# Optimization experiments

Measured on AMD Instinct MI355X. Metric: run time of the kernel, lower is better.

The kernel has to match this reference:

```python
import jax, jax.numpy as jnp
import numpy as np

HEAD_NUM = 16


def setup_inputs() -> dict:
    key = jax.random.key(0)
    k1, k2, k3, k4 = jax.random.split(key, 4)
    B, S, E = 8, 1024, 1024
    inputs = jax.random.normal(k1, (B, S, E), dtype=jnp.float32)
    W_Query = jax.random.normal(k2, (E, E), dtype=jnp.float32) * 0.05
    W_Key = jax.random.normal(k3, (E, E), dtype=jnp.float32) * 0.05
    W_Value = jax.random.normal(k4, (E, E), dtype=jnp.float32) * 0.05
    return {"inputs": inputs, "W_Query": W_Query, "W_Key": W_Key, "W_Value": W_Value}


def reference(inputs, W_Query, W_Key, W_Value):
    B, S, E = inputs.shape
    H = HEAD_NUM
    D = E // H
    # QKV projections: [B,S,E] @ [E,E] -> [B,S,E]
    q = jnp.einsum('bse,ef->bsf', inputs, W_Query).reshape(B, S, H, D)
    k = jnp.einsum('bse,ef->bsf', inputs, W_Key).reshape(B, S, H, D)
    v = jnp.einsum('bse,ef->bsf', inputs, W_Value).reshape(B, S, H, D)
    # NOTE: original has NO 1/sqrt(D) scaling.
    scores = jnp.einsum('bihd,bjhd->bhij', q, k)  # [B,H,S,S]
    att = jax.nn.softmax(scores, axis=-1)
    out = jnp.einsum('bhij,bjhd->bihd', att, v).reshape(B, S, E)
    return jax.nn.relu(out)
```

## Files before the change

kernel.cpp:

```cpp
#include <hip/hip_runtime.h>
#include <cstdint>
#include <cstddef>

#define B_ 8
#define S_ 1024
#define E_ 1024
#define H_ 16
#define D_ 64
#define M_ (B_*S_)

typedef _Float16 f16;
typedef __attribute__((ext_vector_type(8))) _Float16 f16x8;
typedef __attribute__((ext_vector_type(4))) _Float16 f16x4;
typedef __attribute__((ext_vector_type(4))) float  f32x4;
typedef __attribute__((ext_vector_type(16))) float f32x16;
typedef __attribute__((ext_vector_type(4))) int    int4v;
typedef __attribute__((ext_vector_type(2))) int    int2v;

__device__ __forceinline__ f32x4 mfma16(f16x8 a, f16x8 b, f32x4 c) {
  return __builtin_amdgcn_mfma_f32_16x16x32_f16(a, b, c, 0, 0, 0);
}
__device__ __forceinline__ f32x16 mfma32(f16x8 a, f16x8 b, f32x16 c) {
  return __builtin_amdgcn_mfma_f32_32x32x16_f16(a, b, c, 0, 0, 0);
}
__device__ __forceinline__ void gll16(const f16* g, f16* l) {
  __builtin_amdgcn_global_load_lds(
      (const __attribute__((address_space(1))) void*)g,
      (__attribute__((address_space(3))) void*)l, 16, 0, 0);
}
__device__ __forceinline__ int pkrtz(float lo, float hi) {
  return __builtin_bit_cast(int, __builtin_amdgcn_cvt_pkrtz(lo, hi));
}

__global__ __launch_bounds__(256) void presplit_kernel(
    const float* __restrict__ X, f16* __restrict__ Xf) {
  size_t i = ((size_t)blockIdx.x * 256 + threadIdx.x) * 8;
  f32x4 v0 = *(const f32x4*)&X[i];
  f32x4 v1 = *(const f32x4*)&X[i + 4];
  f16x8 hv;
#pragma unroll
  for (int j = 0; j < 4; ++j) {
    hv[j] = (f16)v0[j];
    hv[j + 4] = (f16)v1[j];
  }
  *(f16x8*)&Xf[i] = hv;
}

__global__ __launch_bounds__(512) void wt_conv3_kernel(
    const float* __restrict__ Wq, const float* __restrict__ Wk,
    const float* __restrict__ Wv, f16* __restrict__ oq, f16* __restrict__ ok,
    f16* __restrict__ ov) {
  const float* W = blockIdx.z == 0 ? Wq : (blockIdx.z == 1 ? Wk : Wv);
  f16* o = blockIdx.z == 0 ? oq : (blockIdx.z == 1 ? ok : ov);
  const float scl = blockIdx.z == 0 ? 1.4426950408889634f : 1.0f;
  __shared__ float t[64][65];
  const int f0 = blockIdx.x * 64, e0 = blockIdx.y * 64;
  const int tx = threadIdx.x, ty = threadIdx.y;
#pragma unroll
  for (int j = 0; j < 8; ++j)
    t[ty + 8 * j][tx] = W[(size_t)(e0 + ty + 8 * j) * E_ + f0 + tx];
  __syncthreads();
#pragma unroll
  for (int j = 0; j < 8; ++j)
    o[(size_t)(f0 + ty + 8 * j) * E_ + e0 + tx] =
        (f16)(t[tx][ty + 8 * j] * scl);
}

__global__ __launch_bounds__(256) void gemm_qkv_kernel(
    const f16* __restrict__ Xf,
    const f16* __restrict__ Wq, const f16* __restrict__ Wk,
    const f16* __restrict__ Wv,
    f16* __restrict__ Qf, f16* __restrict__ Kf, f16* __restrict__ Vt) {
  __shared__ f16 sA[128][64], sB[128][64];
  const int bid = blockIdx.x;
  const int xcd = bid & 7, idx = bid >> 3;
  const int mb = xcd * 8 + idx / 24;
  const int nb = idx % 24;
  const int z = nb >> 3;
  const int n0 = (nb & 7) * 128, m0 = mb * 128;
  const f16* __restrict__ Bt = z == 0 ? Wq : (z == 1 ? Wk : Wv);
  const int tid = threadIdx.x;
  const int lane = tid & 63, w = tid >> 6;
  const int wm = (w >> 1) * 64, wn = (w & 1) * 64;
  const int fr = lane & 15, fg = lane >> 4;
  f32x4 acc[4][4] = {};
  for (int k0 = 0; k0 < E_; k0 += 64) {
#pragma unroll
    for (int i = 0; i < 4; ++i) {
      int ci = tid + i * 256;
      int r = ci >> 3, cl = ci & 7;
      int cs = (cl ^ (r & 7)) * 8;
      gll16(Xf + (size_t)(m0 + r) * E_ + k0 + cs, &sA[0][0] + ci * 8);
      gll16(Bt + (size_t)(n0 + r) * E_ + k0 + cs, &sB[0][0] + ci * 8);
    }
    __syncthreads();
#pragma unroll
    for (int kh2 = 0; kh2 < 2; ++kh2) {
      f16x8 ah[4];
#pragma unroll
      for (int mi = 0; mi < 4; ++mi) {
        int rA = wm + mi * 16 + fr;
        ah[mi] = *(const f16x8*)&sA[rA][(((kh2 * 4 + fg) ^ (rA & 7))) * 8];
      }
#pragma unroll
      for (int ni = 0; ni < 4; ++ni) {
        int rB = wn + ni * 16 + fr;
        f16x8 bh = *(const f16x8*)&sB[rB][(((kh2 * 4 + fg) ^ (rB & 7))) * 8];
#pragma unroll
        for (int mi = 0; mi < 4; ++mi)
          acc[mi][ni] = mfma16(ah[mi], bh, acc[mi][ni]);
      }
    }
    __syncthreads();
  }
  if (z < 2) {
    f16* Of = z == 0 ? Qf : Kf;
#pragma unroll
    for (int mi = 0; mi < 4; ++mi)
#pragma unroll
      for (int ni = 0; ni < 4; ++ni)
#pragma unroll
        for (int r = 0; r < 4; ++r) {
          int row = m0 + wm + mi * 16 + (lane >> 4) * 4 + r;
          int col = n0 + wn + ni * 16 + fr;
          int bb = row >> 10, s = row & 1023;
          int hd = col >> 6, d = col & 63;
          Of[((size_t)(bb * H_ + hd) * S_ + s) * D_ + d] = (f16)acc[mi][ni][r];
        }
  } else {
#pragma unroll
    for (int mi = 0; mi < 4; ++mi)
#pragma unroll
      for (int ni = 0; ni < 4; ++ni) {
        int row = m0 + wm + mi * 16 + (lane >> 4) * 4;
        int col = n0 + wn + ni * 16 + fr;
        int bb = row >> 10, s = row & 1023;
        int hd = col >> 6, d = col & 63;
        f16x4 p;
#pragma unroll
        for (int r = 0; r < 4; ++r) p[r] = (f16)acc[mi][ni][r];
        *(f16x4*)&Vt[((size_t)(bb * H_ + hd) * D_ + d) * S_ + s] = p;
      }
  }
}

__global__ __launch_bounds__(256, 4) void attn_kernel(
    const f16* __restrict__ Qf, const f16* __restrict__ Kf,
    const f16* __restrict__ Vt, float* __restrict__ out) {
  __shared__ f16 sK[2][64][64], sV[2][64][64];
  const int bid = blockIdx.x;
  const int bh = (bid & 7) * 16 + (bid >> 6);
  const int qb = (bid >> 3) & 7;
  const int hd = bh & 15, bb = bh >> 4;
  const int tid = threadIdx.x;
  const int lane = tid & 63, w = tid >> 6;
  const int cq = lane & 31, h = lane >> 5;
  const int rsw = cq & 7;
  const size_t base = (size_t)bh * (S_ * D_);
  const f16* Qf_p = Qf + base;
  const f16* Kf_p = Kf + base;
  const f16* Vt_p = Vt + base;
  const int q0 = qb * 128 + w * 32;

  f16x8 qh_[4];
#pragma unroll
  for (int ks = 0; ks < 4; ++ks)
    qh_[ks] = *(const f16x8*)&Qf_p[(size_t)(q0 + cq) * D_ + ks * 16 + 8 * h];

  f16x8 ones;
#pragma unroll
  for (int j = 0; j < 8; ++j) ones[j] = (f16)1.0f;

  float m_run;
  f32x16 O[2] = {}, Ol = {};
  f16x8 pf[4];

#define STAGE(buf, kb)                                                        \
  {                                                                           \
    _Pragma("unroll")                                                         \
    for (int half = 0; half < 2; ++half) {                                    \
      int ci = tid + half * 256;                                              \
      int row = ci >> 3, cl = ci & 7;                                         \
      int cs = cl ^ (row & 7);                                                \
      gll16(Kf_p + (size_t)((kb) + row) * D_ + cs * 8, &sK[buf][0][0] + ci * 8); \
      gll16(Vt_p + (size_t)row * S_ + (kb) + cs * 8, &sV[buf][0][0] + ci * 8);   \
    }                                                                         \
  }

#define QKT(scv, bufi)                                                        \
  {                                                                           \
    _Pragma("unroll")                                                         \
    for (int f = 0; f < 2; ++f) {                                             \
      _Pragma("unroll")                                                       \
      for (int ks = 0; ks < 4; ++ks) {                                        \
        int cc = ((2 * ks + h) ^ rsw) * 8;                                    \
        f16x8 kv = *(const f16x8*)&sK[bufi][f * 32 + cq][cc];                 \
        scv[f] = mfma32(kv, qh_[ks], scv[f]);                                 \
      }                                                                       \
    }                                                                         \
  }

#define MAXTREE(pm, scv)                                                      \
  {                                                                           \
    float t4[4];                                                              \
    _Pragma("unroll")                                                         \
    for (int i = 0; i < 4; ++i) {                                             \
      float a = fmaxf(fmaxf(scv[0][i], scv[0][i + 4]),                        \
                      fmaxf(scv[0][i + 8], scv[0][i + 12]));                  \
      float b = fmaxf(fmaxf(scv[1][i], scv[1][i + 4]),                        \
                      fmaxf(scv[1][i + 8], scv[1][i + 12]));                  \
      t4[i] = fmaxf(a, b);                                                    \
    }                                                                         \
    pm = fmaxf(fmaxf(t4[0], t4[1]), fmaxf(t4[2], t4[3]));                     \
    pm = fmaxf(pm, __shfl_xor(pm, 32));                                       \
  }

#define PFBUILD(scv)                                                          \
  {                                                                           \
    _Pragma("unroll")                                                         \
    for (int f = 0; f < 2; ++f) {                                             \
      _Pragma("unroll")                                                       \
      for (int ksl = 0; ksl < 2; ++ksl) {                                     \
        int b0 = 8 * ksl;                                                     \
        int a1 = pkrtz(scv[f][b0 + 0], scv[f][b0 + 1]);                       \
        int b1 = pkrtz(scv[f][b0 + 4], scv[f][b0 + 5]);                       \
        int2v r1 = __builtin_amdgcn_permlane32_swap(a1, b1, false, false);    \
        int a2 = pkrtz(scv[f][b0 + 2], scv[f][b0 + 3]);                       \
        int b2 = pkrtz(scv[f][b0 + 6], scv[f][b0 + 7]);                       \
        int2v r2 = __builtin_amdgcn_permlane32_swap(a2, b2, false, false);    \
        int4v wd;                                                             \
        wd[0] = r1[0]; wd[1] = r2[0]; wd[2] = r1[1]; wd[3] = r2[1];           \
        pf[2 * f + ksl] = __builtin_bit_cast(f16x8, wd);                      \
      }                                                                       \
    }                                                                         \
  }

#define PVT(bufi)                                                             \
  {                                                                           \
    _Pragma("unroll")                                                         \
    for (int ks = 0; ks < 4; ++ks) {                                          \
      int cc = ((2 * ks + h) ^ rsw) * 8;                                      \
      _Pragma("unroll")                                                       \
      for (int df = 0; df < 2; ++df) {                                        \
        f16x8 vf = *(const f16x8*)&sV[bufi][df * 32 + cq][cc];                \
        O[df] = mfma32(vf, pf[ks], O[df]);                                    \
      }                                                                       \
      Ol = mfma32(ones, pf[ks], Ol);                                          \
    }                                                                         \
  }

  STAGE(0, 0);
  asm volatile("s_waitcnt vmcnt(0)" ::: "memory");
  __builtin_amdgcn_sched_barrier(0);
  __builtin_amdgcn_s_barrier();
  STAGE(1, 64);
  {
    f32x16 sc[2] = {};
    __builtin_amdgcn_s_setprio(1);
    QKT(sc, 0);
    __builtin_amdgcn_s_setprio(0);
    float pm;
    MAXTREE(pm, sc);
    m_run = pm;
#pragma unroll
    for (int f = 0; f < 2; ++f)
#pragma unroll
      for (int r = 0; r < 16; ++r)
        sc[f][r] = __builtin_amdgcn_exp2f(sc[f][r] - pm);
    PFBUILD(sc);
    __builtin_amdgcn_s_setprio(1);
    PVT(0);
    __builtin_amdgcn_s_setprio(0);
  }
  asm volatile("s_waitcnt vmcnt(0)" ::: "memory");
  __builtin_amdgcn_sched_barrier(0);
  __builtin_amdgcn_s_barrier();

  for (int t = 1; t < 16; ++t) {
    const int cur = t & 1;
    if (t < 15) STAGE(cur ^ 1, (t + 1) * 64);

    f32x16 sc[2];
#pragma unroll
    for (int f = 0; f < 2; ++f)
#pragma unroll
      for (int r = 0; r < 16; ++r) sc[f][r] = -m_run;
    __builtin_amdgcn_s_setprio(1);
    QKT(sc, cur);
    __builtin_amdgcn_s_setprio(0);

#pragma unroll
    for (int f = 0; f < 2; ++f)
#pragma unroll
      for (int r = 0; r < 16; ++r)
        sc[f][r] = __builtin_amdgcn_exp2f(sc[f][r]);

    float pm;
    MAXTREE(pm, sc);
    if (__any(pm > 2048.f)) {
      float pmx = fmaxf(pm, 1.0f);
      float scl = 1.0f / pmx;
      m_run += __builtin_amdgcn_logf(pmx);
#pragma unroll
      for (int f = 0; f < 2; ++f)
#pragma unroll
        for (int r = 0; r < 16; ++r) sc[f][r] *= scl;
#pragma unroll
      for (int df = 0; df < 2; ++df)
#pragma unroll
        for (int i = 0; i < 16; ++i) O[df][i] *= scl;
#pragma unroll
      for (int i = 0; i < 16; ++i) Ol[i] *= scl;
    }

    PFBUILD(sc);
    __builtin_amdgcn_s_setprio(1);
    PVT(cur);
    __builtin_amdgcn_s_setprio(0);

    asm volatile("s_waitcnt vmcnt(0)" ::: "memory");
    __builtin_amdgcn_sched_barrier(0);
    __builtin_amdgcn_s_barrier();
  }

  float inv = 1.0f / Ol[0];
  int s = q0 + cq;
  float* orow = out + ((size_t)bb * S_ + s) * E_ + hd * 64;
#pragma unroll
  for (int df = 0; df < 2; ++df)
#pragma unroll
    for (int g = 0; g < 4; ++g) {
      f32x4 vv;
#pragma unroll
      for (int j = 0; j < 4; ++j)
        vv[j] = fmaxf(O[df][4 * g + j] * inv, 0.f);
      *(f32x4*)&orow[df * 32 + 8 * g + 4 * h] = vv;
    }
}

extern "C" void kernel_launch(void* const* d_in, const int* in_sizes, int n_in,
                              void* d_out, int out_size, void* d_ws, size_t ws_size,
                              hipStream_t stream) {
  const float* X  = (const float*)d_in[0];
  const float* Wq = (const float*)d_in[1];
  const float* Wk = (const float*)d_in[2];
  const float* Wv = (const float*)d_in[3];
  float* out = (float*)d_out;
  char* ws = (char*)d_ws;

  const size_t WSZ = (size_t)E_ * E_ * sizeof(f16);
  const size_t QSZ = (size_t)M_ * E_ * sizeof(f16);
  f16* Wqf = (f16*)(ws);
  f16* Wkf = (f16*)(ws + WSZ);
  f16* Wvf = (f16*)(ws + 2 * WSZ);
  char* p = ws + 3 * WSZ;
  f16* Xf = (f16*)(p);
  f16* Qf = (f16*)(p + QSZ);
  f16* Kf = (f16*)(p + 2 * QSZ);
  f16* Vt = (f16*)(p + 3 * QSZ);

  presplit_kernel<<<4096, 256, 0, stream>>>(X, Xf);
  wt_conv3_kernel<<<dim3(16, 16, 3), dim3(64, 8), 0, stream>>>(
      Wq, Wk, Wv, Wqf, Wkf, Wvf);

  gemm_qkv_kernel<<<1536, 256, 0, stream>>>(
      Xf, Wqf, Wkf, Wvf, Qf, Kf, Vt);

  attn_kernel<<<1024, 256, 0, stream>>>(Qf, Kf, Vt, out);
}
```

Before: 132.7 us.

## Load K/V fragments directly from global memory and compute row sums with VALU

The attention kernel drops its double-buffered LDS staging of K and V tiles and the block barriers, and each lane now loads its MFMA K and V fragments straight from global memory (relying on cache reuse across the four waves). The row-sum is computed with VALU adds plus a cross-half shuffle instead of an extra MFMA against a ones vector, which removes one MFMA per k-step. Launch bounds no longer request 4 blocks per SM. The change trades LDS traffic and synchronisation for redundant global/L2 loads and less latency hiding, since loads are issued right before use with no prefetch.

```diff
diff --git a/kernel.cpp b/kernel.cpp
--- a/kernel.cpp
+++ b/kernel.cpp
@@ -144,60 +144,51 @@
   }
 }
 
-__global__ __launch_bounds__(256, 4) void attn_kernel(
+__global__ __launch_bounds__(256) void attn_kernel(
     const f16* __restrict__ Qf, const f16* __restrict__ Kf,
     const f16* __restrict__ Vt, float* __restrict__ out) {
-  __shared__ f16 sK[2][64][64], sV[2][64][64];
   const int bid = blockIdx.x;
   const int bh = (bid & 7) * 16 + (bid >> 6);
   const int qb = (bid >> 3) & 7;
   const int hd = bh & 15, bb = bh >> 4;
-  const int tid = threadIdx.x;
-  const int lane = tid & 63, w = tid >> 6;
+  const int lane = threadIdx.x & 63, w = threadIdx.x >> 6;
   const int cq = lane & 31, h = lane >> 5;
-  const int rsw = cq & 7;
   const size_t base = (size_t)bh * (S_ * D_);
-  const f16* Qf_p = Qf + base;
-  const f16* Kf_p = Kf + base;
-  const f16* Vt_p = Vt + base;
+  const f16* Qp = Qf + base;
+  const f16* Kp = Kf + base + (size_t)cq * D_ + 8 * h;
+  const f16* Vp = Vt + base + (size_t)cq * S_ + 8 * h;
   const int q0 = qb * 128 + w * 32;
 
   f16x8 qh_[4];
 #pragma unroll
   for (int ks = 0; ks < 4; ++ks)
-    qh_[ks] = *(const f16x8*)&Qf_p[(size_t)(q0 + cq) * D_ + ks * 16 + 8 * h];
-
-  f16x8 ones;
-#pragma unroll
-  for (int j = 0; j < 8; ++j) ones[j] = (f16)1.0f;
-
-  float m_run;
-  f32x16 O[2] = {}, Ol = {};
+    qh_[ks] = *(const f16x8*)&Qp[(size_t)(q0 + cq) * D_ + ks * 16 + 8 * h];
+
+  float m_run, l_run;
+  f32x16 O[2] = {};
   f16x8 pf[4];
 
-#define STAGE(buf, kb)                                                        \
-  {                                                                           \
-    _Pragma("unroll")                                                         \
-    for (int half = 0; half < 2; ++half) {                                    \
-      int ci = tid + half * 256;                                              \
-      int row = ci >> 3, cl = ci & 7;                                         \
-      int cs = cl ^ (row & 7);                                                \
-      gll16(Kf_p + (size_t)((kb) + row) * D_ + cs * 8, &sK[buf][0][0] + ci * 8); \
-      gll16(Vt_p + (size_t)row * S_ + (kb) + cs * 8, &sV[buf][0][0] + ci * 8);   \
-    }                                                                         \
-  }
-
-#define QKT(scv, bufi)                                                        \
+#define QKT(scv, t)                                                           \
   {                                                                           \
     _Pragma("unroll")                                                         \
     for (int f = 0; f < 2; ++f) {                                             \
+      f16x8 kv[4];                                                            \
       _Pragma("unroll")                                                       \
-      for (int ks = 0; ks < 4; ++ks) {                                        \
-        int cc = ((2 * ks + h) ^ rsw) * 8;                                    \
-        f16x8 kv = *(const f16x8*)&sK[bufi][f * 32 + cq][cc];                 \
-        scv[f] = mfma32(kv, qh_[ks], scv[f]);                                 \
-      }                                                                       \
-    }                                                                         \
+      for (int ks = 0; ks < 4; ++ks)                                          \
+        kv[ks] = *(const f16x8*)&Kp[((t) * 64 + f * 32) * D_ + ks * 16];      \
+      __builtin_amdgcn_s_setprio(1);                                          \
+      _Pragma("unroll")                                                       \
+      for (int ks = 0; ks < 4; ++ks)                                          \
+        scv[f] = mfma32(kv[ks], qh_[ks], scv[f]);                             \
+      __builtin_amdgcn_s_setprio(0);                                          \
+    }                                                                         \
+  }
+
+#define LOADV(vfv, t, df)                                                     \
+  {                                                                           \
+    _Pragma("unroll")                                                         \
+    for (int ks = 0; ks < 4; ++ks)                                            \
+      vfv[ks] = *(const f16x8*)&Vp[(size_t)(df) * 32 * S_ + (t) * 64 + ks * 16]; \
   }
 
 #define MAXTREE(pm, scv)                                                      \
@@ -213,6 +204,23 @@
     }                                                                         \
     pm = fmaxf(fmaxf(t4[0], t4[1]), fmaxf(t4[2], t4[3]));                     \
     pm = fmaxf(pm, __shfl_xor(pm, 32));                                       \
+  }
+
+#define ROWSUM(rs, scv)                                                       \
+  {                                                                           \
+    float rs0 = 0.f, rs1 = 0.f, rs2 = 0.f, rs3 = 0.f;                         \
+    _Pragma("unroll")                                                         \
+    for (int f = 0; f < 2; ++f) {                                             \
+      _Pragma("unroll")                                                       \
+      for (int r4 = 0; r4 < 4; ++r4) {                                        \
+        rs0 += scv[f][4 * r4 + 0];                                            \
+        rs1 += scv[f][4 * r4 + 1];                                            \
+        rs2 += scv[f][4 * r4 + 2];                                            \
+        rs3 += scv[f][4 * r4 + 3];                                            \
+      }                                                                       \
+    }                                                                         \
+    rs = (rs0 + rs1) + (rs2 + rs3);                                           \
+    rs += __shfl_xor(rs, 32);                                                 \
   }
 
 #define PFBUILD(scv)                                                          \
@@ -235,30 +243,23 @@
     }                                                                         \
   }
 
-#define PVT(bufi)                                                             \
-  {                                                                           \
+#define PVT(t)                                                                \
+  {                                                                           \
+    f16x8 vf0[4], vf1[4];                                                     \
+    LOADV(vf0, t, 0);                                                         \
+    LOADV(vf1, t, 1);                                                         \
+    __builtin_amdgcn_s_setprio(1);                                            \
     _Pragma("unroll")                                                         \
     for (int ks = 0; ks < 4; ++ks) {                                          \
-      int cc = ((2 * ks + h) ^ rsw) * 8;                                      \
-      _Pragma("unroll")                                                       \
-      for (int df = 0; df < 2; ++df) {                                        \
-        f16x8 vf = *(const f16x8*)&sV[bufi][df * 32 + cq][cc];                \
-        O[df] = mfma32(vf, pf[ks], O[df]);                                    \
-      }                                                                       \
-      Ol = mfma32(ones, pf[ks], Ol);                                          \
-    }                                                                         \
-  }
-
-  STAGE(0, 0);
-  asm volatile("s_waitcnt vmcnt(0)" ::: "memory");
-  __builtin_amdgcn_sched_barrier(0);
-  __builtin_amdgcn_s_barrier();
-  STAGE(1, 64);
+      O[0] = mfma32(vf0[ks], pf[ks], O[0]);                                   \
+      O[1] = mfma32(vf1[ks], pf[ks], O[1]);                                   \
+    }                                                                         \
+    __builtin_amdgcn_s_setprio(0);                                            \
+  }
+
   {
     f32x16 sc[2] = {};
-    __builtin_amdgcn_s_setprio(1);
     QKT(sc, 0);
-    __builtin_amdgcn_s_setprio(0);
     float pm;
     MAXTREE(pm, sc);
     m_run = pm;
@@ -267,27 +268,20 @@
 #pragma unroll
       for (int r = 0; r < 16; ++r)
         sc[f][r] = __builtin_amdgcn_exp2f(sc[f][r] - pm);
+    float rs;
+    ROWSUM(rs, sc);
+    l_run = rs;
     PFBUILD(sc);
-    __builtin_amdgcn_s_setprio(1);
     PVT(0);
-    __builtin_amdgcn_s_setprio(0);
-  }
-  asm volatile("s_waitcnt vmcnt(0)" ::: "memory");
-  __builtin_amdgcn_sched_barrier(0);
-  __builtin_amdgcn_s_barrier();
+  }
 
   for (int t = 1; t < 16; ++t) {
-    const int cur = t & 1;
-    if (t < 15) STAGE(cur ^ 1, (t + 1) * 64);
-
     f32x16 sc[2];
 #pragma unroll
     for (int f = 0; f < 2; ++f)
 #pragma unroll
       for (int r = 0; r < 16; ++r) sc[f][r] = -m_run;
-    __builtin_amdgcn_s_setprio(1);
-    QKT(sc, cur);
-    __builtin_amdgcn_s_setprio(0);
+    QKT(sc, t);
 
 #pragma unroll
     for (int f = 0; f < 2; ++f)
@@ -301,6 +295,7 @@
       float pmx = fmaxf(pm, 1.0f);
       float scl = 1.0f / pmx;
       m_run += __builtin_amdgcn_logf(pmx);
+      l_run *= scl;
 #pragma unroll
       for (int f = 0; f < 2; ++f)
 #pragma unroll
@@ -309,21 +304,16 @@
       for (int df = 0; df < 2; ++df)
 #pragma unroll
         for (int i = 0; i < 16; ++i) O[df][i] *= scl;
-#pragma unroll
-      for (int i = 0; i < 16; ++i) Ol[i] *= scl;
     }
 
+    float rs;
+    ROWSUM(rs, sc);
+    l_run += rs;
     PFBUILD(sc);
-    __builtin_amdgcn_s_setprio(1);
-    PVT(cur);
-    __builtin_amdgcn_s_setprio(0);
-
-    asm volatile("s_waitcnt vmcnt(0)" ::: "memory");
-    __builtin_amdgcn_sched_barrier(0);
-    __builtin_amdgcn_s_barrier();
-  }
-
-  float inv = 1.0f / Ol[0];
+    PVT(t);
+  }
+
+  float inv = 1.0f / l_run;
   int s = q0 + cq;
   float* orow = out + ((size_t)bb * S_ + s) * E_ + hd * 64;
 #pragma unroll
```

Measured after the change: 206.6 us. 55.7% more time.

## Double-buffer LDS tiles in QKV projection GEMM to overlap loads with MFMA

Applied to the files above, without the earlier changes.

Converts the QKV GEMM's single LDS buffers into ping-pong buffers, issuing the global-to-LDS loads for the next k-tile before computing on the current one. Each iteration now ends with one vmcnt wait and a barrier instead of the two __syncthreads around the load. This aims to hide global load latency behind MFMA work. LDS use per block doubles to 64KB, which may lower occupancy, and the synchronization relies on the explicit waitcnt ordering being correct.

```diff
diff --git a/kernel.cpp b/kernel.cpp
--- a/kernel.cpp
+++ b/kernel.cpp
@@ -71,7 +71,7 @@
     const f16* __restrict__ Wq, const f16* __restrict__ Wk,
     const f16* __restrict__ Wv,
     f16* __restrict__ Qf, f16* __restrict__ Kf, f16* __restrict__ Vt) {
-  __shared__ f16 sA[128][64], sB[128][64];
+  __shared__ f16 sA[2][128][64], sB[2][128][64];
   const int bid = blockIdx.x;
   const int xcd = bid & 7, idx = bid >> 3;
   const int mb = xcd * 8 + idx / 24;
@@ -84,34 +84,47 @@
   const int wm = (w >> 1) * 64, wn = (w & 1) * 64;
   const int fr = lane & 15, fg = lane >> 4;
   f32x4 acc[4][4] = {};
+
+#define GSTAGE(buf, k0s)                                                      \
+  {                                                                           \
+    _Pragma("unroll")                                                         \
+    for (int i = 0; i < 4; ++i) {                                             \
+      int ci = tid + i * 256;                                                 \
+      int r = ci >> 3, cl = ci & 7;                                           \
+      int cs = (cl ^ (r & 7)) * 8;                                            \
+      gll16(Xf + (size_t)(m0 + r) * E_ + (k0s) + cs, &sA[buf][0][0] + ci * 8);\
+      gll16(Bt + (size_t)(n0 + r) * E_ + (k0s) + cs, &sB[buf][0][0] + ci * 8);\
+    }                                                                         \
+  }
+
+  GSTAGE(0, 0);
+  asm volatile("s_waitcnt vmcnt(0)" ::: "memory");
+  __builtin_amdgcn_sched_barrier(0);
+  __builtin_amdgcn_s_barrier();
+
   for (int k0 = 0; k0 < E_; k0 += 64) {
-#pragma unroll
-    for (int i = 0; i < 4; ++i) {
-      int ci = tid + i * 256;
-      int r = ci >> 3, cl = ci & 7;
-      int cs = (cl ^ (r & 7)) * 8;
-      gll16(Xf + (size_t)(m0 + r) * E_ + k0 + cs, &sA[0][0] + ci * 8);
-      gll16(Bt + (size_t)(n0 + r) * E_ + k0 + cs, &sB[0][0] + ci * 8);
-    }
-    __syncthreads();
+    const int cur = (k0 >> 6) & 1;
+    if (k0 + 64 < E_) GSTAGE(cur ^ 1, k0 + 64);
 #pragma unroll
     for (int kh2 = 0; kh2 < 2; ++kh2) {
       f16x8 ah[4];
 #pragma unroll
       for (int mi = 0; mi < 4; ++mi) {
         int rA = wm + mi * 16 + fr;
-        ah[mi] = *(const f16x8*)&sA[rA][(((kh2 * 4 + fg) ^ (rA & 7))) * 8];
+        ah[mi] = *(const f16x8*)&sA[cur][rA][(((kh2 * 4 + fg) ^ (rA & 7))) * 8];
       }
 #pragma unroll
       for (int ni = 0; ni < 4; ++ni) {
         int rB = wn + ni * 16 + fr;
-        f16x8 bh = *(const f16x8*)&sB[rB][(((kh2 * 4 + fg) ^ (rB & 7))) * 8];
+        f16x8 bh = *(const f16x8*)&sB[cur][rB][(((kh2 * 4 + fg) ^ (rB & 7))) * 8];
 #pragma unroll
         for (int mi = 0; mi < 4; ++mi)
           acc[mi][ni] = mfma16(ah[mi], bh, acc[mi][ni]);
       }
     }
-    __syncthreads();
+    asm volatile("s_waitcnt vmcnt(0)" ::: "memory");
+    __builtin_amdgcn_sched_barrier(0);
+    __builtin_amdgcn_s_barrier();
   }
   if (z < 2) {
     f16* Of = z == 0 ? Qf : Kf;
```

New measurement: 136.7 us. 1.03x slower.

## Rewrite QKV GEMM as 256x256 tile with 8 waves and double-buffered LDS

Applied to the files above, without the earlier changes.

Replaces the 128x128, 4-wave QKV projection GEMM with a 256x256 tile computed by 8 waves over double-buffered shared memory. Global-to-LDS loads for the next K step are interleaved with the MFMA phases, using explicit vmcnt waits, barriers and s_setprio, so load latency overlaps compute. The larger tile raises operand reuse and cuts the number of blocks from 1536 to 384. In exchange it uses 128 KB of LDS per block and more accumulator registers, which limits occupancy, and fewer blocks may not fill every CU evenly.

```diff
diff --git a/kernel.cpp b/kernel.cpp
--- a/kernel.cpp
+++ b/kernel.cpp
@@ -66,74 +66,118 @@
         (f16)(t[tx][ty + 8 * j] * scl);
 }
 
-__global__ __launch_bounds__(256) void gemm_qkv_kernel(
+__global__ __launch_bounds__(512) void gemm_qkv8_kernel(
     const f16* __restrict__ Xf,
     const f16* __restrict__ Wq, const f16* __restrict__ Wk,
     const f16* __restrict__ Wv,
     f16* __restrict__ Qf, f16* __restrict__ Kf, f16* __restrict__ Vt) {
-  __shared__ f16 sA[128][64], sB[128][64];
+  __shared__ f16 sA[2][256][64], sB[2][256][64];
   const int bid = blockIdx.x;
   const int xcd = bid & 7, idx = bid >> 3;
-  const int mb = xcd * 8 + idx / 24;
-  const int nb = idx % 24;
-  const int z = nb >> 3;
-  const int n0 = (nb & 7) * 128, m0 = mb * 128;
+  const int mb = xcd * 4 + idx / 12;
+  const int nt = idx % 12;
+  const int z = nt >> 2;
+  const int m0 = mb * 256;
+  const int n0 = (nt & 3) * 256;
   const f16* __restrict__ Bt = z == 0 ? Wq : (z == 1 ? Wk : Wv);
   const int tid = threadIdx.x;
   const int lane = tid & 63, w = tid >> 6;
-  const int wm = (w >> 1) * 64, wn = (w & 1) * 64;
+  const int wr = (w >> 2) * 128, wc = (w & 3) * 64;
   const int fr = lane & 15, fg = lane >> 4;
-  f32x4 acc[4][4] = {};
-  for (int k0 = 0; k0 < E_; k0 += 64) {
-#pragma unroll
-    for (int i = 0; i < 4; ++i) {
-      int ci = tid + i * 256;
-      int r = ci >> 3, cl = ci & 7;
-      int cs = (cl ^ (r & 7)) * 8;
-      gll16(Xf + (size_t)(m0 + r) * E_ + k0 + cs, &sA[0][0] + ci * 8);
-      gll16(Bt + (size_t)(n0 + r) * E_ + k0 + cs, &sB[0][0] + ci * 8);
+
+  f32x4 acc[8][4] = {};
+
+#define GS_A(slot, kt, hh)                                                    \
+  { _Pragma("unroll") for (int j = 0; j < 2; ++j) {                           \
+      int ci = tid + j * 512;                                                 \
+      int r = ci >> 3, cl = ci & 7;                                           \
+      int cs = (cl ^ (r & 7)) * 8;                                            \
+      gll16(Xf + (size_t)(m0 + (hh) * 128 + r) * E_ + (kt) * 64 + cs,         \
+            &sA[slot][(hh) * 128][0] + ci * 8); } }
+#define GS_B(slot, kt, hh)                                                    \
+  { _Pragma("unroll") for (int j = 0; j < 2; ++j) {                           \
+      int ci = tid + j * 512;                                                 \
+      int r = ci >> 3, cl = ci & 7;                                           \
+      int cs = (cl ^ (r & 7)) * 8;                                            \
+      gll16(Bt + (size_t)(n0 + (hh) * 128 + r) * E_ + (kt) * 64 + cs,         \
+            &sB[slot][(hh) * 128][0] + ci * 8); } }
+#define RD_B(slot)                                                            \
+  { _Pragma("unroll") for (int ni = 0; ni < 4; ++ni)                          \
+      _Pragma("unroll") for (int ks = 0; ks < 2; ++ks) {                      \
+        int rB = wc + ni * 16 + fr;                                           \
+        bf[ni][ks] =                                                          \
+            *(const f16x8*)&sB[slot][rB][(((ks * 4 + fg) ^ (rB & 7))) * 8]; } }
+#define RD_A2(slot, q)                                                        \
+  { _Pragma("unroll") for (int dm = 0; dm < 2; ++dm)                          \
+      _Pragma("unroll") for (int ks = 0; ks < 2; ++ks) {                      \
+        int rA = wr + ((q) * 2 + dm) * 16 + fr;                               \
+        af[dm][ks] =                                                          \
+            *(const f16x8*)&sA[slot][rA][(((ks * 4 + fg) ^ (rA & 7))) * 8]; } }
+#define MMQ(q)                                                                \
+  { __builtin_amdgcn_s_setprio(1);                                            \
+    _Pragma("unroll") for (int ni = 0; ni < 4; ++ni)                          \
+      _Pragma("unroll") for (int ks = 0; ks < 2; ++ks)                        \
+        _Pragma("unroll") for (int dm = 0; dm < 2; ++dm)                      \
+          acc[(q) * 2 + dm][ni] =                                             \
+              mfma16(af[dm][ks], bf[ni][ks], acc[(q) * 2 + dm][ni]);          \
+    __builtin_amdgcn_s_setprio(0); }
+#define GBAR()                                                                \
+  { __builtin_amdgcn_sched_barrier(0);                                        \
+    __builtin_amdgcn_s_barrier();                                             \
+    __builtin_amdgcn_sched_barrier(0); }
+
+  GS_A(0, 0, 0); GS_A(0, 0, 1);
+  GS_B(0, 0, 0); GS_B(0, 0, 1);
+  GS_B(1, 1, 0); GS_B(1, 1, 1);
+  asm volatile("s_waitcnt vmcnt(4)" ::: "memory");
+  GBAR();
+
+  for (int k = 0; k < 16; ++k) {
+    const int slot = k & 1;
+    f16x8 bf[4][2], af[2][2];
+    RD_B(slot);
+    RD_A2(slot, 0);
+    if (k < 15) GS_A(slot ^ 1, k + 1, 0);
+    MMQ(0);
+    RD_A2(slot, 1);
+    if (k < 15) GS_A(slot ^ 1, k + 1, 1);
+    MMQ(1);
+    GBAR();
+    RD_A2(slot, 2);
+    if (k < 14) GS_B(slot, k + 2, 0);
+    MMQ(2);
+    RD_A2(slot, 3);
+    if (k < 14) GS_B(slot, k + 2, 1);
+    MMQ(3);
+    if (k < 14) {
+      asm volatile("s_waitcnt vmcnt(4)" ::: "memory");
+    } else {
+      asm volatile("s_waitcnt vmcnt(0)" ::: "memory");
     }
-    __syncthreads();
-#pragma unroll
-    for (int kh2 = 0; kh2 < 2; ++kh2) {
-      f16x8 ah[4];
-#pragma unroll
-      for (int mi = 0; mi < 4; ++mi) {
-        int rA = wm + mi * 16 + fr;
-        ah[mi] = *(const f16x8*)&sA[rA][(((kh2 * 4 + fg) ^ (rA & 7))) * 8];
-      }
-#pragma unroll
-      for (int ni = 0; ni < 4; ++ni) {
-        int rB = wn + ni * 16 + fr;
-        f16x8 bh = *(const f16x8*)&sB[rB][(((kh2 * 4 + fg) ^ (rB & 7))) * 8];
-#pragma unroll
-        for (int mi = 0; mi < 4; ++mi)
-          acc[mi][ni] = mfma16(ah[mi], bh, acc[mi][ni]);
-      }
-    }
-    __syncthreads();
-  }
+    GBAR();
+  }
+
   if (z < 2) {
     f16* Of = z == 0 ? Qf : Kf;
 #pragma unroll
-    for (int mi = 0; mi < 4; ++mi)
+    for (int mi = 0; mi < 8; ++mi)
 #pragma unroll
       for (int ni = 0; ni < 4; ++ni)
 #pragma unroll
         for (int r = 0; r < 4; ++r) {
-          int row = m0 + wm + mi * 16 + (lane >> 4) * 4 + r;
-          int col = n0 + wn + ni * 16 + fr;
+          int row = m0 + wr + mi * 16 + fg * 4 + r;
+          int col = n0 + wc + ni * 16 + fr;
           int bb = row >> 10, s = row & 1023;
           int hd = col >> 6, d = col & 63;
           Of[((size_t)(bb * H_ + hd) * S_ + s) * D_ + d] = (f16)acc[mi][ni][r];
         }
   } else {
 #pragma unroll
-    for (int mi = 0; mi < 4; ++mi)
+    for (int mi = 0; mi < 8; ++mi)
 #pragma unroll
       for (int ni = 0; ni < 4; ++ni) {
-        int row = m0 + wm + mi * 16 + (lane >> 4) * 4;
-        int col = n0 + wn + ni * 16 + fr;
+        int row = m0 + wr + mi * 16 + fg * 4;
+        int col = n0 + wc + ni * 16 + fr;
         int bb = row >> 10, s = row & 1023;
         int hd = col >> 6, d = col & 63;
         f16x4 p;
@@ -142,6 +186,12 @@
         *(f16x4*)&Vt[((size_t)(bb * H_ + hd) * D_ + d) * S_ + s] = p;
       }
   }
+#undef GS_A
+#undef GS_B
+#undef RD_B
+#undef RD_A2
+#undef MMQ
+#undef GBAR
 }
 
 __global__ __launch_bounds__(256, 4) void attn_kernel(
@@ -363,7 +413,7 @@
   wt_conv3_kernel<<<dim3(16, 16, 3), dim3(64, 8), 0, stream>>>(
       Wq, Wk, Wv, Wqf, Wkf, Wvf);
 
-  gemm_qkv_kernel<<<1536, 256, 0, stream>>>(
+  gemm_qkv8_kernel<<<384, 512, 0, stream>>>(
       Xf, Wqf, Wkf, Wvf, Qf, Kf, Vt);
 
   attn_kernel<<<1024, 256, 0, stream>>>(Qf, Kf, Vt, out);
```

Result: slower. 147.7 us (+11.4%).
